# Kernel optimization log

Hardware: AMD Instinct MI355X
Metric: run time of the kernel (lower is better)

## Reference

```python
import jax, jax.numpy as jnp
import numpy as np

NUM_USR = 8192
H = 256  # NUM_SOURCE == H (feature dim of y_a); NUM_TARGET = 256


def setup_inputs() -> dict:
    key = jax.random.key(0)
    k1, k2, k3, k4 = jax.random.split(key, 4)
    return {
        "y_a": jax.random.normal(k1, (NUM_USR, H), dtype=jnp.float32),
        "y_b": jax.random.normal(k2, (NUM_USR, H), dtype=jnp.float32),
        "W": jax.random.normal(k3, (H, H), dtype=jnp.float32) * (1.0 / np.sqrt(H)),
        "b": jax.random.normal(k4, (H,), dtype=jnp.float32) * 0.01,
    }


def reference(y_a, y_b, W, b):
    # Linear: proj[j] = W @ y_b[j] + b   (torch nn.Linear convention)
    proj = jnp.einsum("jt,st->js", y_b, W) + b          # [num_usr, H]
    # torch loop computes score[i, j] = y_a[i] . proj[j], replicated H times
    # then averaged: out[i, k] = (1/H) * sum_j sigmoid(score[i, j])
    scores = jnp.einsum("ih,jh->ij", y_a, proj)          # [num_usr, num_usr]
    s = jnp.sum(jax.nn.sigmoid(scores), axis=1) / y_a.shape[1]  # [num_usr]
    return jnp.broadcast_to(s[:, None], y_a.shape)       # [num_usr, H]
```

## Files before the change

### kernel.cpp

```cpp
#include <hip/hip_runtime.h>

#define NUSR 8192
#define HDIM 256

typedef __attribute__((ext_vector_type(8))) __bf16 bf16x8;
typedef __attribute__((ext_vector_type(4))) float f32x4;

union frag_u { bf16x8 v; unsigned short u[8]; unsigned int d[4]; };

__device__ __forceinline__ unsigned int f2bf(float f) {
  unsigned u = __builtin_bit_cast(unsigned, f);
  u += 0x7FFFu + ((u >> 16) & 1u);
  return u >> 16;
}
__device__ __forceinline__ unsigned int f2bf2(float lo, float hi) {
  return f2bf(lo) | (f2bf(hi) << 16);
}
__device__ __forceinline__ float sigmoidf_fast(float x) {
  float e = __builtin_amdgcn_exp2f(x * -1.44269504088896340736f);
  return __builtin_amdgcn_rcpf(1.0f + e);
}


__global__ __launch_bounds__(256) void k1_fused(
    const float* __restrict__ ya, const float* __restrict__ yb,
    const float* __restrict__ W, const float* __restrict__ bvec,
    unsigned short* __restrict__ yabf, unsigned short* __restrict__ PX,
    float* __restrict__ svec)
{
  const int b   = blockIdx.x;
  const int tid = threadIdx.x;

  if (b < 256) {
    const int lane = tid & 63;
    const int w    = tid >> 6;
    const int q    = lane >> 4;
    const int i    = lane & 15;

    frag_u B[2][8];
#pragma unroll
    for (int g = 0; g < 2; ++g) {
      const float* ybrow = yb + (size_t)(b * 32 + g * 16 + i) * HDIM;
#pragma unroll
      for (int kb = 0; kb < 8; ++kb) {
        float4 v0 = *(const float4*)&ybrow[kb * 32 + q * 8];
        float4 v1 = *(const float4*)&ybrow[kb * 32 + q * 8 + 4];
        B[g][kb].d[0] = f2bf2(v0.x, v0.y); B[g][kb].d[1] = f2bf2(v0.z, v0.w);
        B[g][kb].d[2] = f2bf2(v1.x, v1.y); B[g][kb].d[3] = f2bf2(v1.z, v1.w);
      }
    }

#pragma unroll
    for (int t = 0; t < 4; ++t) {
      const int st = w * 4 + t;
      f32x4 acc[2] = {{0.f,0.f,0.f,0.f},{0.f,0.f,0.f,0.f}};
#pragma unroll
      for (int kb = 0; kb < 8; ++kb) {
        const float* wr = W + (size_t)(st * 16 + i) * HDIM + kb * 32 + q * 8;
        float4 w0 = *(const float4*)wr;
        float4 w1 = *(const float4*)(wr + 4);
        frag_u Af;
        Af.d[0] = f2bf2(w0.x, w0.y); Af.d[1] = f2bf2(w0.z, w0.w);
        Af.d[2] = f2bf2(w1.x, w1.y); Af.d[3] = f2bf2(w1.z, w1.w);
#pragma unroll
        for (int g = 0; g < 2; ++g)
          acc[g] = __builtin_amdgcn_mfma_f32_16x16x32_bf16(Af.v, B[g][kb].v, acc[g], 0, 0, 0);
      }
      float4 bias = *(const float4*)&bvec[st * 16 + q * 4];
#pragma unroll
      for (int g = 0; g < 2; ++g) {
        const int jg = b * 2 + g;
        unsigned v0 = f2bf2(acc[g][0] + bias.x, acc[g][1] + bias.y);
        unsigned v1 = f2bf2(acc[g][2] + bias.z, acc[g][3] + bias.w);
        size_t off = (size_t)jg * 4096 + (size_t)(st >> 1) * 512
                   + (size_t)(((st & 1) << 1) | (q >> 1)) * 128 + i * 8 + ((q & 1) * 4);
        *(uint2*)(PX + off) = make_uint2(v0, v1);
      }
    }
  } else {
    const int id = (b - 256) * 256 + tid;
    const float4* src = (const float4*)ya;
    uint4* dst = (uint4*)yabf;
#pragma unroll
    for (int u = 0; u < 4; ++u) {
      int d = id + u * 65536;
      float4 a = src[d * 2];
      float4 c = src[d * 2 + 1];
      uint4 o = { f2bf2(a.x, a.y), f2bf2(a.z, a.w),
                  f2bf2(c.x, c.y), f2bf2(c.z, c.w) };
      dst[d] = o;
    }
    if (b == 511) {
      float4 z = {0.f, 0.f, 0.f, 0.f};
      float4* sv = (float4*)svec;
#pragma unroll
      for (int u = 0; u < 8; ++u) sv[u * 256 + tid] = z;
    }
  }
}

__global__ __launch_bounds__(256, 2) void k2_score(
    const unsigned short* __restrict__ yabf, const unsigned short* __restrict__ PX,
    float* __restrict__ svec)
{
  __shared__ __align__(16) unsigned short bs[2][16384];
  const int tid  = threadIdx.x;
  const int lane = tid & 63;
  const int w    = tid >> 6;
  const int quad = lane >> 4;
  const int l15  = lane & 15;

  const int bid = blockIdx.x;
  const int xcd = bid & 7;
  const int k   = bid >> 3;
  const int by  = xcd * 2 + (k >> 5);
  const int bx  = k & 31;

  const int rbase = bx * 256 + w * 64;
  const int cg16  = by * 32;

  const unsigned short* psrc = PX + (size_t)cg16 * 4096;

#define STAGE(B, T)                                                          \
  do {                                                                       \
    const unsigned short* _src = psrc + (size_t)(T) * 16384;                 \
    unsigned short* _dst = &bs[(B)][0];                                      \
    _Pragma("unroll")                                                        \
    for (int p = 0; p < 8; ++p) {                                            \
      int c = p * 256 + tid;                                                 \
      __builtin_amdgcn_global_load_lds(                                      \
          (const __attribute__((address_space(1))) unsigned int*)(const void*)(_src + c * 8), \
          (__attribute__((address_space(3))) unsigned int*)(void*)(_dst + c * 8), \
          16, 0, 0);                                                         \
    }                                                                        \
  } while (0)

  STAGE(0, 0);

  frag_u A[4][8];
#pragma unroll
  for (int g = 0; g < 4; ++g) {
    const unsigned short* src = yabf + (size_t)(rbase + g * 16 + l15) * HDIM;
#pragma unroll
    for (int kb = 0; kb < 8; ++kb)
      A[g][kb].v = *(const bf16x8*)&src[kb * 32 + quad * 8];
  }
#pragma unroll
  for (int g = 0; g < 4; ++g)
#pragma unroll
    for (int kb = 0; kb < 8; ++kb)
      asm volatile("" : "+v"(A[g][kb].v));

  float rs[4][4] = {{0.f,0.f,0.f,0.f},{0.f,0.f,0.f,0.f},
                    {0.f,0.f,0.f,0.f},{0.f,0.f,0.f,0.f}};

#define MFMA_PHASE(ACC, BUF, P)                                              \
  do {                                                                       \
    _Pragma("unroll")                                                        \
    for (int g = 0; g < 4; ++g) ACC[g] = (f32x4){0.f, 0.f, 0.f, 0.f};        \
    __builtin_amdgcn_s_setprio(1);                                           \
    _Pragma("unroll")                                                        \
    for (int kb = 0; kb < 8; ++kb) {                                         \
      bf16x8 bfrag = *(const bf16x8*)&BUF[(P) * 4096 + kb * 512 + lane * 8]; \
      _Pragma("unroll")                                                      \
      for (int g = 0; g < 4; ++g)                                            \
        ACC[g] = __builtin_amdgcn_mfma_f32_16x16x32_bf16(                    \
            A[g][kb].v, bfrag, ACC[g], 0, 0, 0);                             \
    }                                                                        \
    __builtin_amdgcn_s_setprio(0);                                           \
  } while (0)

#define SIG(ACC)                                                             \
  do {                                                                       \
    _Pragma("unroll")                                                        \
    for (int g = 0; g < 4; ++g)                                              \
      _Pragma("unroll")                                                      \
      for (int r = 0; r < 4; ++r)                                            \
        rs[g][r] += sigmoidf_fast(ACC[g][r]);                                \
  } while (0)

  for (int t = 0; t < 8; ++t) {
    asm volatile("s_waitcnt vmcnt(0)" ::: "memory");
    asm volatile("s_barrier" ::: "memory");
    if (t < 7)
      STAGE((t + 1) & 1, t + 1);

    const unsigned short* buf = &bs[t & 1][0];
    f32x4 accA[4], accB[4];
    MFMA_PHASE(accA, buf, 0);
    MFMA_PHASE(accB, buf, 1);
    SIG(accA);
    MFMA_PHASE(accA, buf, 2);
    SIG(accB);
    MFMA_PHASE(accB, buf, 3);
    SIG(accA);
    SIG(accB);
  }
#undef STAGE
#undef MFMA_PHASE
#undef SIG

#pragma unroll
  for (int off = 1; off < 16; off <<= 1)
#pragma unroll
    for (int g = 0; g < 4; ++g)
#pragma unroll
      for (int r = 0; r < 4; ++r)
        rs[g][r] += __shfl_xor(rs[g][r], off, 64);

  if (l15 == 0) {
#pragma unroll
    for (int g = 0; g < 4; ++g)
#pragma unroll
      for (int r = 0; r < 4; ++r)
        atomicAdd(&svec[rbase + g * 16 + quad * 4 + r], rs[g][r]);
  }
}

__global__ __launch_bounds__(256) void k3_bcast(
    const float* __restrict__ svec, float* __restrict__ out)
{
  int idx = blockIdx.x * 256 + threadIdx.x;
  int row = idx >> 6;
  float v = svec[row] * (1.0f / 256.0f);
  float4 o = {v, v, v, v};
  ((float4*)out)[idx] = o;
}

extern "C" void kernel_launch(void* const* d_in, const int* in_sizes, int n_in,
                              void* d_out, int out_size, void* d_ws, size_t ws_size,
                              hipStream_t stream) {
  (void)in_sizes; (void)n_in; (void)out_size;
  const float* ya = (const float*)d_in[0];
  const float* yb = (const float*)d_in[1];
  const float* W  = (const float*)d_in[2];
  const float* bv = (const float*)d_in[3];
  float* out = (float*)d_out;

  char* ws = (char*)d_ws;
  unsigned short *PX, *yabf;
  float* svec;
  const size_t need = (8ull << 20) + (32ull << 10);
  if (ws_size >= need) {
    PX   = (unsigned short*)ws;
    yabf = (unsigned short*)(ws + (4 << 20));
    svec = (float*)(ws + (8 << 20));
  } else {
    PX   = (unsigned short*)d_out;
    yabf = (unsigned short*)((char*)d_out + (4 << 20));
    svec = (float*)ws;
  }

  k1_fused<<<512, 256, 0, stream>>>(ya, yb, W, bv, yabf, PX, svec);
  k2_score<<<512, 256, 0, stream>>>(yabf, PX, svec);
  k3_bcast<<<2048, 256, 0, stream>>>(svec, out);
}
```

Before: 121.6 us.

## Software-pipeline sigmoid of previous tile into current MFMA phase

Each MFMA phase now also applies the sigmoid to the previous phase's accumulator, interleaving 2 sigmoids with every 4 MFMAs. It uses sched_group_barrier hints to force the MFMA and VALU interleave, and the setprio calls are removed. The accumulator is primed with a large negative value so the first sigmoid adds zero, and an epilogue handles the last tile. The aim is to hide the sigmoid VALU and transcendental work under the matrix-core latency, at the cost of keeping both accumulator sets live across the loop and relying on the scheduling hints.

```diff
diff --git a/kernel.cpp b/kernel.cpp
--- a/kernel.cpp
+++ b/kernel.cpp
@@ -154,29 +154,29 @@
   float rs[4][4] = {{0.f,0.f,0.f,0.f},{0.f,0.f,0.f,0.f},
                     {0.f,0.f,0.f,0.f},{0.f,0.f,0.f,0.f}};
 
-#define MFMA_PHASE(ACC, BUF, P)                                              \
+  f32x4 accA[4], accB[4];
+#pragma unroll
+  for (int g = 0; g < 4; ++g) accB[g] = (f32x4){-1e30f, -1e30f, -1e30f, -1e30f};
+
+#define PHASE(ACCC, ACCP, BUF, P)                                            \
   do {                                                                       \
     _Pragma("unroll")                                                        \
-    for (int g = 0; g < 4; ++g) ACC[g] = (f32x4){0.f, 0.f, 0.f, 0.f};        \
-    __builtin_amdgcn_s_setprio(1);                                           \
+    for (int g = 0; g < 4; ++g) ACCC[g] = (f32x4){0.f, 0.f, 0.f, 0.f};       \
     _Pragma("unroll")                                                        \
     for (int kb = 0; kb < 8; ++kb) {                                         \
       bf16x8 bfrag = *(const bf16x8*)&BUF[(P) * 4096 + kb * 512 + lane * 8]; \
       _Pragma("unroll")                                                      \
       for (int g = 0; g < 4; ++g)                                            \
-        ACC[g] = __builtin_amdgcn_mfma_f32_16x16x32_bf16(                    \
-            A[g][kb].v, bfrag, ACC[g], 0, 0, 0);                             \
+        ACCC[g] = __builtin_amdgcn_mfma_f32_16x16x32_bf16(                   \
+            A[g][kb].v, bfrag, ACCC[g], 0, 0, 0);                            \
+      _Pragma("unroll")                                                      \
+      for (int s = 0; s < 2; ++s) {                                          \
+        const int m = kb * 2 + s;                                            \
+        rs[m >> 2][m & 3] += sigmoidf_fast(ACCP[m >> 2][m & 3]);             \
+      }                                                                      \
+      __builtin_amdgcn_sched_group_barrier(0x008, 4, 0);        \
+      __builtin_amdgcn_sched_group_barrier(0x002, 10, 0);       \
     }                                                                        \
-    __builtin_amdgcn_s_setprio(0);                                           \
-  } while (0)
-
-#define SIG(ACC)                                                             \
-  do {                                                                       \
-    _Pragma("unroll")                                                        \
-    for (int g = 0; g < 4; ++g)                                              \
-      _Pragma("unroll")                                                      \
-      for (int r = 0; r < 4; ++r)                                            \
-        rs[g][r] += sigmoidf_fast(ACC[g][r]);                                \
   } while (0)
 
   for (int t = 0; t < 8; ++t) {
@@ -186,19 +186,17 @@
       STAGE((t + 1) & 1, t + 1);
 
     const unsigned short* buf = &bs[t & 1][0];
-    f32x4 accA[4], accB[4];
-    MFMA_PHASE(accA, buf, 0);
-    MFMA_PHASE(accB, buf, 1);
-    SIG(accA);
-    MFMA_PHASE(accA, buf, 2);
-    SIG(accB);
-    MFMA_PHASE(accB, buf, 3);
-    SIG(accA);
-    SIG(accB);
+    PHASE(accA, accB, buf, 0);
+    PHASE(accB, accA, buf, 1);
+    PHASE(accA, accB, buf, 2);
+    PHASE(accB, accA, buf, 3);
   }
 #undef STAGE
-#undef MFMA_PHASE
-#undef SIG
+#undef PHASE
+
+#pragma unroll
+  for (int m = 0; m < 16; ++m)
+    rs[m >> 2][m & 3] += sigmoidf_fast(accB[m >> 2][m & 3]);
 
 #pragma unroll
   for (int off = 1; off < 16; off <<= 1)
```

New measurement: 123.1 us. About the same (+1.3%).
